# Kernel tuning notes

Measured on AMD Instinct MI355X. Metric: run time of the kernel, lower is better.

The kernel has to match this reference:

```python
import jax, jax.numpy as jnp
import numpy as np

EMB = 1024
HEADS = 16
HEAD_DIM = EMB // HEADS  # 64


def setup_inputs() -> dict:
    key = jax.random.key(0)
    ks = jax.random.split(key, 11)
    B, S = 2, 2048
    scale = 1.0 / np.sqrt(EMB)
    inp = {
        "xv": jax.random.normal(ks[0], (B, S, EMB), jnp.float32),
        "xk": jax.random.normal(ks[1], (B, S, EMB), jnp.float32),
        "xq": jax.random.normal(ks[2], (B, S, EMB), jnp.float32),
        "Wq": jax.random.normal(ks[3], (EMB, EMB), jnp.float32) * scale,
        "bq": jax.random.normal(ks[4], (EMB,), jnp.float32) * 0.01,
        "Wk": jax.random.normal(ks[5], (EMB, EMB), jnp.float32) * scale,
        "bk": jax.random.normal(ks[6], (EMB,), jnp.float32) * 0.01,
        "Wv": jax.random.normal(ks[7], (EMB, EMB), jnp.float32) * scale,
        "bv": jax.random.normal(ks[8], (EMB,), jnp.float32) * 0.01,
        "Wo": jax.random.normal(ks[9], (EMB, EMB), jnp.float32) * scale,
        "bo": jax.random.normal(ks[10], (EMB,), jnp.float32) * 0.01,
    }
    return inp


def reference(xv, xk, xq, Wq, bq, Wk, bk, Wv, bv, Wo, bo):
    B, S, E = xq.shape
    H, D = HEADS, HEAD_DIM
    # projections (x @ W + b), split into heads: [B,S,H,D]
    Q = (xq @ Wq + bq).reshape(B, S, H, D)
    K = (xk @ Wk + bk).reshape(B, S, H, D)
    V = (xv @ Wv + bv).reshape(B, S, H, D)
    # scaled dot-product attention per head (vectorized over heads)
    scores = jnp.einsum("bqhd,bkhd->bhqk", Q, K) / jnp.sqrt(jnp.float32(D))
    attn = jax.nn.softmax(scores, axis=-1)
    ctx = jnp.einsum("bhqk,bkhd->bqhd", attn, V).reshape(B, S, E)
    return ctx @ Wo + bo
```

## Files before the change

### kernel.cpp

```cpp
#include <hip/hip_runtime.h>
#include <hip/hip_bf16.h>

typedef __hip_bfloat16 bf16;
typedef __attribute__((ext_vector_type(8))) short short8;
typedef __attribute__((ext_vector_type(4))) short short4v;
typedef __attribute__((ext_vector_type(4))) float floatx4;

#define MFMA16 __builtin_amdgcn_mfma_f32_16x16x32_bf16


__device__ __forceinline__ void gl16(const void* g, void* l) {
    __builtin_amdgcn_global_load_lds(
        (const __attribute__((address_space(1))) void*)g,
        (__attribute__((address_space(3))) void*)l, 16, 0, 0);
}

__global__ __launch_bounds__(256) void wtrans_k(const float* __restrict__ w0,
                                                const float* __restrict__ w1,
                                                const float* __restrict__ w2,
                                                const float* __restrict__ w3,
                                                bf16* __restrict__ dst) {
    const float* srcs[4] = {w0, w1, w2, w3};
    const float* src = srcs[blockIdx.z];
    bf16* d = dst + (size_t)blockIdx.z * 1024 * 1024;
    __shared__ float t[32][33];
    int tx = threadIdx.x, ty = threadIdx.y;
    int x0 = blockIdx.x * 32, y0 = blockIdx.y * 32;
#pragma unroll
    for (int i = 0; i < 4; i++)
        t[ty + i * 8][tx] = src[(size_t)(y0 + ty + i * 8) * 1024 + x0 + tx];
    __syncthreads();
#pragma unroll
    for (int i = 0; i < 4; i++)
        d[(size_t)(x0 + ty + i * 8) * 1024 + y0 + tx] =
            __float2bfloat16(t[tx][ty + i * 8]);
}

__global__ __launch_bounds__(256) void xcast_k(const float* __restrict__ x0,
                                               const float* __restrict__ x1,
                                               const float* __restrict__ x2,
                                               bf16* __restrict__ dst) {
    const float* srcs[3] = {x0, x1, x2};
    const float* src = srcs[blockIdx.y];
    bf16* d = dst + (size_t)blockIdx.y * (4096 * 1024);
    size_t i = (size_t)blockIdx.x * 256 + threadIdx.x;
    const float4* s4 = (const float4*)src + i * 2;
    float4 a = s4[0], b = s4[1];
    union { __hip_bfloat162 h2[4]; short8 s; } pk;
    pk.h2[0] = __float22bfloat162_rn(make_float2(a.x, a.y));
    pk.h2[1] = __float22bfloat162_rn(make_float2(a.z, a.w));
    pk.h2[2] = __float22bfloat162_rn(make_float2(b.x, b.y));
    pk.h2[3] = __float22bfloat162_rn(make_float2(b.z, b.w));
    *(short8*)&d[i * 8] = pk.s;
}

__global__ __launch_bounds__(256) void qkv_k(const bf16* __restrict__ xb,
                                             const bf16* __restrict__ wt,
                                             const float* __restrict__ bq,
                                             const float* __restrict__ bk,
                                             const float* __restrict__ bv,
                                             bf16* __restrict__ Qw,
                                             bf16* __restrict__ Kw,
                                             bf16* __restrict__ Vt) {
    __shared__ __align__(16) bf16 lA[2][128 * 32];
    __shared__ __align__(16) bf16 lB[2][128 * 32];
    int z = blockIdx.z;
    const bf16* A = xb + (size_t)z * (4096 * 1024);
    const bf16* Bt = wt + (size_t)z * (1024 * 1024);
    const float* bias = (z == 0) ? bq : (z == 1) ? bk : bv;
    int m0 = blockIdx.x * 128, n0 = blockIdx.y * 128;
    int tid = threadIdx.x, wave = tid >> 6, lane = tid & 63;
    int lm = lane & 15, quad = lane >> 4;
    int wm = wave >> 1, wn = wave & 1;
    int swb = quad ^ ((lm >> 1) & 3);

    floatx4 acc[4][4];
#pragma unroll
    for (int i = 0; i < 4; i++)
#pragma unroll
        for (int j = 0; j < 4; j++) acc[i][j] = (floatx4){0.f, 0.f, 0.f, 0.f};

    auto stage = [&](int bufi, int kt) {
#pragma unroll
        for (int q2 = 0; q2 < 2; q2++) {
            int slot0 = wave * 128 + q2 * 64;
            int r = (slot0 + lane) >> 2;
            int c = (lane & 3) ^ ((r >> 1) & 3);
            gl16(&A[(size_t)(m0 + r) * 1024 + kt * 32 + c * 8],
                 &lA[bufi][slot0 * 8]);
            gl16(&Bt[(size_t)(n0 + r) * 1024 + kt * 32 + c * 8],
                 &lB[bufi][slot0 * 8]);
        }
    };

    stage(0, 0);
    __syncthreads();

    for (int kt = 0; kt < 32; kt++) {
        int cur = kt & 1;
        if (kt < 31) stage(cur ^ 1, kt + 1);

        short8 af[4], bfr[4];
#pragma unroll
        for (int ms = 0; ms < 4; ms++) {
            int r = wm * 64 + ms * 16 + lm;
            af[ms] = *(const short8*)&lA[cur][(r * 4 + swb) * 8];
        }
#pragma unroll
        for (int ns = 0; ns < 4; ns++) {
            int r = wn * 64 + ns * 16 + lm;
            bfr[ns] = *(const short8*)&lB[cur][(r * 4 + swb) * 8];
        }
#pragma unroll
        for (int ms = 0; ms < 4; ms++)
#pragma unroll
            for (int ns = 0; ns < 4; ns++)
                acc[ms][ns] = MFMA16(af[ms], bfr[ns], acc[ms][ns], 0, 0, 0);
        __syncthreads();
    }

    bf16* dstQK = (z == 0) ? Qw : Kw;
    float scale = (z == 0) ? 0.125f * 1.44269504f : 1.0f;
#pragma unroll
    for (int ms = 0; ms < 4; ms++) {
        int rowb = m0 + wm * 64 + ms * 16 + quad * 4;
        int bb = rowb >> 11, s0 = rowb & 2047;
#pragma unroll
        for (int ns = 0; ns < 4; ns++) {
            int col = n0 + wn * 64 + ns * 16 + lm;
            float bvv = bias[col];
            int hh = col >> 6, d = col & 63;
            if (z < 2) {
#pragma unroll
                for (int rr = 0; rr < 4; rr++) {
                    float v = (acc[ms][ns][rr] + bvv) * scale;
                    dstQK[((((size_t)bb * 16 + hh) * 2048 + s0 + rr) << 6) + d] =
                        __float2bfloat16(v);
                }
            } else {
                short4v pk;
#pragma unroll
                for (int rr = 0; rr < 4; rr++) {
                    bf16 h = __float2bfloat16(acc[ms][ns][rr] + bvv);
                    pk[rr] = *(short*)&h;
                }
                *(short4v*)&Vt[((((size_t)bb * 16 + hh) * 64 + d) << 11) + s0] = pk;
            }
        }
    }
}

__global__ __launch_bounds__(256) void outproj_k(const bf16* __restrict__ ctx,
                                                 const bf16* __restrict__ wot,
                                                 const float* __restrict__ bo,
                                                 float* __restrict__ out) {
    __shared__ __align__(16) bf16 lA[2][128 * 32];
    __shared__ __align__(16) bf16 lB[2][64 * 32];
    int m0 = blockIdx.x * 128, n0 = blockIdx.y * 64;
    int tid = threadIdx.x, wave = tid >> 6, lane = tid & 63;
    int lm = lane & 15, quad = lane >> 4;
    int wm = wave >> 1, wn = wave & 1;
    int swb = quad ^ ((lm >> 1) & 3);

    floatx4 acc[4][2];
#pragma unroll
    for (int i = 0; i < 4; i++)
#pragma unroll
        for (int j = 0; j < 2; j++) acc[i][j] = (floatx4){0.f, 0.f, 0.f, 0.f};

    auto stage = [&](int bufi, int kt) {
#pragma unroll
        for (int q2 = 0; q2 < 2; q2++) {
            int slot0 = wave * 128 + q2 * 64;
            int r = (slot0 + lane) >> 2;
            int c = (lane & 3) ^ ((r >> 1) & 3);
            gl16(&ctx[(size_t)(m0 + r) * 1024 + kt * 32 + c * 8],
                 &lA[bufi][slot0 * 8]);
        }
        {
            int slot0 = wave * 64;
            int r = (slot0 + lane) >> 2;
            int c = (lane & 3) ^ ((r >> 1) & 3);
            gl16(&wot[(size_t)(n0 + r) * 1024 + kt * 32 + c * 8],
                 &lB[bufi][slot0 * 8]);
        }
    };

    stage(0, 0);
    __syncthreads();

    for (int kt = 0; kt < 32; kt++) {
        int cur = kt & 1;
        if (kt < 31) stage(cur ^ 1, kt + 1);

        short8 af[4], bfr[2];
#pragma unroll
        for (int ms = 0; ms < 4; ms++) {
            int r = wm * 64 + ms * 16 + lm;
            af[ms] = *(const short8*)&lA[cur][(r * 4 + swb) * 8];
        }
#pragma unroll
        for (int ns = 0; ns < 2; ns++) {
            int r = wn * 32 + ns * 16 + lm;
            bfr[ns] = *(const short8*)&lB[cur][(r * 4 + swb) * 8];
        }
#pragma unroll
        for (int ms = 0; ms < 4; ms++)
#pragma unroll
            for (int ns = 0; ns < 2; ns++)
                acc[ms][ns] = MFMA16(af[ms], bfr[ns], acc[ms][ns], 0, 0, 0);
        __syncthreads();
    }

#pragma unroll
    for (int ms = 0; ms < 4; ms++) {
        int rowb = m0 + wm * 64 + ms * 16 + quad * 4;
#pragma unroll
        for (int ns = 0; ns < 2; ns++) {
            int col = n0 + wn * 32 + ns * 16 + lm;
            float bvv = bo[col];
#pragma unroll
            for (int rr = 0; rr < 4; rr++)
                out[(size_t)(rowb + rr) * 1024 + col] = acc[ms][ns][rr] + bvv;
        }
    }
}

__global__ __launch_bounds__(256) void attn_k(const bf16* __restrict__ Q,
                                              const bf16* __restrict__ K,
                                              const bf16* __restrict__ Vt,
                                              bf16* __restrict__ ctx) {
    __shared__ __align__(16) bf16 lK[2][64 * 64];
    __shared__ __align__(16) bf16 lV[2][64 * 64];
    __shared__ __align__(16) bf16 lP[64 * 64];
    int bh = blockIdx.x, qt = blockIdx.y;
    int b = bh >> 4, h = bh & 15;
    const bf16* Qh = Q + (size_t)bh * (2048 * 64);
    const bf16* Kh = K + (size_t)bh * (2048 * 64);
    const bf16* Vh = Vt + (size_t)bh * (64 * 2048);
    int tid = threadIdx.x, wave = tid >> 6, lane = tid & 63;
    int lm = lane & 15, quad = lane >> 4;
    int s7 = lm & 7;

    int qrow = qt * 64 + wave * 16 + lm;
    short8 qf0 = *(const short8*)&Qh[(size_t)qrow * 64 + quad * 8];
    short8 qf1 = *(const short8*)&Qh[(size_t)qrow * 64 + 32 + quad * 8];

    short8 onesf;
#pragma unroll
    for (int i = 0; i < 8; i++) onesf[i] = (short)0x3F80;

    floatx4 o[4];
#pragma unroll
    for (int i = 0; i < 4; i++) o[i] = (floatx4){0.f, 0.f, 0.f, 0.f};
    floatx4 accL = (floatx4){0.f, 0.f, 0.f, 0.f};

    auto stage = [&](int bufi, int kt) {
#pragma unroll
        for (int q2 = 0; q2 < 2; q2++) {
            int slot0 = wave * 128 + q2 * 64;
            int r = (slot0 + lane) >> 3;
            int c = (lane & 7) ^ (r & 7);
            gl16(&Kh[(size_t)(kt * 64 + r) * 64 + c * 8], &lK[bufi][slot0 * 8]);
            gl16(&Vh[(size_t)r * 2048 + kt * 64 + c * 8], &lV[bufi][slot0 * 8]);
        }
    };

    stage(0, 0);
    __syncthreads();

    char* lProw = (char*)lP + (wave * 16 + lm) * 128;

    for (int kt = 0; kt < 32; kt++) {
        int cur = kt & 1;
        if (kt < 31) stage(cur ^ 1, kt + 1);

        floatx4 s[4];
#pragma unroll
        for (int i = 0; i < 4; i++) s[i] = (floatx4){0.f, 0.f, 0.f, 0.f};
#pragma unroll
        for (int ns = 0; ns < 4; ns++) {
            int r = ns * 16 + lm;
            short8 kf0 = *(const short8*)&lK[cur][(r * 8 + (quad ^ s7)) * 8];
            short8 kf1 = *(const short8*)&lK[cur][(r * 8 + ((4 + quad) ^ s7)) * 8];
            s[ns] = MFMA16(kf0, qf0, s[ns], 0, 0, 0);
            s[ns] = MFMA16(kf1, qf1, s[ns], 0, 0, 0);
        }

#pragma unroll
        for (int ns = 0; ns < 4; ns++) {
            float p0 = __builtin_amdgcn_exp2f(s[ns][0]);
            float p1 = __builtin_amdgcn_exp2f(s[ns][1]);
            float p2 = __builtin_amdgcn_exp2f(s[ns][2]);
            float p3 = __builtin_amdgcn_exp2f(s[ns][3]);
            union { __hip_bfloat162 h2[2]; short4v s4; } pk;
            pk.h2[0] = __float22bfloat162_rn(make_float2(p0, p1));
            pk.h2[1] = __float22bfloat162_rn(make_float2(p2, p3));
            int sw = (2 * ns + (quad >> 1)) ^ s7;
            *(short4v*)(lProw + sw * 16 + (quad & 1) * 8) = pk.s4;
        }

#pragma unroll
        for (int kk = 0; kk < 2; kk++) {
            int c2 = (kk * 4 + quad) ^ s7;
            short8 pf = *(const short8*)(lProw + c2 * 16);
            accL = MFMA16(pf, onesf, accL, 0, 0, 0);
#pragma unroll
            for (int ns = 0; ns < 4; ns++) {
                int r = ns * 16 + lm;
                short8 vf = *(const short8*)&lV[cur][(r * 8 + ((kk * 4 + quad) ^ s7)) * 8];
                o[ns] = MFMA16(pf, vf, o[ns], 0, 0, 0);
            }
        }
        __syncthreads();
    }

    float inv[4];
#pragma unroll
    for (int rr = 0; rr < 4; rr++) inv[rr] = 1.f / accL[rr];

#pragma unroll
    for (int ns = 0; ns < 4; ns++) {
        int e = h * 64 + ns * 16 + lm;
#pragma unroll
        for (int rr = 0; rr < 4; rr++) {
            int srow = qt * 64 + wave * 16 + quad * 4 + rr;
            ctx[(size_t)(b * 2048 + srow) * 1024 + e] =
                __float2bfloat16(o[ns][rr] * inv[rr]);
        }
    }
}

extern "C" void kernel_launch(void* const* d_in, const int* in_sizes, int n_in,
                              void* d_out, int out_size, void* d_ws, size_t ws_size,
                              hipStream_t stream) {
    const float* xv = (const float*)d_in[0];
    const float* xk = (const float*)d_in[1];
    const float* xq = (const float*)d_in[2];
    const float* Wq = (const float*)d_in[3];
    const float* bq = (const float*)d_in[4];
    const float* Wk = (const float*)d_in[5];
    const float* bk = (const float*)d_in[6];
    const float* Wv = (const float*)d_in[7];
    const float* bv = (const float*)d_in[8];
    const float* Wo = (const float*)d_in[9];
    const float* bo = (const float*)d_in[10];
    float* out = (float*)d_out;
    bf16* ws = (bf16*)d_ws;

    const size_t MB1 = 1024 * 1024;
    bf16* wt  = ws;
    bf16* Qw  = ws + 4 * MB1;
    bf16* Kw  = ws + 8 * MB1;
    bf16* Vt  = ws + 12 * MB1;
    bf16* ctx = ws + 16 * MB1;
    bf16* xb  = ws + 20 * MB1;

    hipLaunchKernelGGL(wtrans_k, dim3(32, 32, 4), dim3(32, 8), 0, stream,
                       Wq, Wk, Wv, Wo, wt);

    hipLaunchKernelGGL(xcast_k, dim3(2048, 3), dim3(256), 0, stream,
                       xq, xk, xv, xb);

    hipLaunchKernelGGL(qkv_k, dim3(32, 8, 3), dim3(256), 0, stream,
                       xb, wt, bq, bk, bv, Qw, Kw, Vt);

    hipLaunchKernelGGL(attn_k, dim3(32, 32), dim3(256), 0, stream, Qw, Kw, Vt, ctx);

    hipLaunchKernelGGL(outproj_k, dim3(32, 16), dim3(256), 0, stream,
                       ctx, wt + 3 * MB1, bo, out);
}
```

Before: 235.1 us.

## Use raw barriers with partial vmcnt waits to overlap prefetch and MFMA compute

```diff
diff --git a/kernel.cpp b/kernel.cpp
--- a/kernel.cpp
+++ b/kernel.cpp
@@ -7,6 +7,8 @@
 typedef __attribute__((ext_vector_type(4))) float floatx4;
 
 #define MFMA16 __builtin_amdgcn_mfma_f32_16x16x32_bf16
+#define BARRIER __builtin_amdgcn_s_barrier
+#define SCHEDB0() __builtin_amdgcn_sched_barrier(0)
 
 
 __device__ __forceinline__ void gl16(const void* g, void* l) {
@@ -93,13 +95,7 @@
         }
     };
 
-    stage(0, 0);
-    __syncthreads();
-
-    for (int kt = 0; kt < 32; kt++) {
-        int cur = kt & 1;
-        if (kt < 31) stage(cur ^ 1, kt + 1);
-
+    auto compute = [&](int cur) {
         short8 af[4], bfr[4];
 #pragma unroll
         for (int ms = 0; ms < 4; ms++) {
@@ -116,8 +112,23 @@
 #pragma unroll
             for (int ns = 0; ns < 4; ns++)
                 acc[ms][ns] = MFMA16(af[ms], bfr[ns], acc[ms][ns], 0, 0, 0);
-        __syncthreads();
-    }
+    };
+
+    stage(0, 0);
+    for (int kt = 0; kt < 31; kt++) {
+        int cur = kt & 1;
+        BARRIER();
+        stage(cur ^ 1, kt + 1);
+        asm volatile("s_waitcnt vmcnt(4)" ::: "memory");
+        BARRIER();
+        SCHEDB0();
+        compute(cur);
+    }
+    BARRIER();
+    asm volatile("s_waitcnt vmcnt(0)" ::: "memory");
+    BARRIER();
+    SCHEDB0();
+    compute(1);
 
     bf16* dstQK = (z == 0) ? Qw : Kw;
     float scale = (z == 0) ? 0.125f * 1.44269504f : 1.0f;
@@ -186,13 +197,7 @@
         }
     };
 
-    stage(0, 0);
-    __syncthreads();
-
-    for (int kt = 0; kt < 32; kt++) {
-        int cur = kt & 1;
-        if (kt < 31) stage(cur ^ 1, kt + 1);
-
+    auto compute = [&](int cur) {
         short8 af[4], bfr[2];
 #pragma unroll
         for (int ms = 0; ms < 4; ms++) {
@@ -209,8 +214,23 @@
 #pragma unroll
             for (int ns = 0; ns < 2; ns++)
                 acc[ms][ns] = MFMA16(af[ms], bfr[ns], acc[ms][ns], 0, 0, 0);
-        __syncthreads();
-    }
+    };
+
+    stage(0, 0);
+    for (int kt = 0; kt < 31; kt++) {
+        int cur = kt & 1;
+        BARRIER();
+        stage(cur ^ 1, kt + 1);
+        asm volatile("s_waitcnt vmcnt(3)" ::: "memory");
+        BARRIER();
+        SCHEDB0();
+        compute(cur);
+    }
+    BARRIER();
+    asm volatile("s_waitcnt vmcnt(0)" ::: "memory");
+    BARRIER();
+    SCHEDB0();
+    compute(1);
 
 #pragma unroll
     for (int ms = 0; ms < 4; ms++) {
@@ -266,15 +286,9 @@
         }
     };
 
-    stage(0, 0);
-    __syncthreads();
-
     char* lProw = (char*)lP + (wave * 16 + lm) * 128;
 
-    for (int kt = 0; kt < 32; kt++) {
-        int cur = kt & 1;
-        if (kt < 31) stage(cur ^ 1, kt + 1);
-
+    auto compute = [&](int cur) {
         floatx4 s[4];
 #pragma unroll
         for (int i = 0; i < 4; i++) s[i] = (floatx4){0.f, 0.f, 0.f, 0.f};
@@ -312,8 +326,23 @@
                 o[ns] = MFMA16(pf, vf, o[ns], 0, 0, 0);
             }
         }
-        __syncthreads();
-    }
+    };
+
+    stage(0, 0);
+    for (int kt = 0; kt < 31; kt++) {
+        int cur = kt & 1;
+        BARRIER();
+        stage(cur ^ 1, kt + 1);
+        asm volatile("s_waitcnt vmcnt(4)" ::: "memory");
+        BARRIER();
+        SCHEDB0();
+        compute(cur);
+    }
+    BARRIER();
+    asm volatile("s_waitcnt vmcnt(0)" ::: "memory");
+    BARRIER();
+    SCHEDB0();
+    compute(1);
 
     float inv[4];
 #pragma unroll
```

After: 228.1 us. 1.03x faster.
